# Optimization experiments

Measured on AMD Instinct MI355X. Metric: run time of the kernel, lower is better.

## Reference

```python
import jax, jax.numpy as jnp
import numpy as np

D = 1024
N_PASSES = 2


def _hadamard(d):
    # Sylvester construction: d must be a power of 2
    H = np.array([[1.0]], dtype=np.float32)
    while H.shape[0] < d:
        H = np.block([[H, H], [H, -H]])
    return H


def setup_inputs() -> dict:
    key = jax.random.key(0)
    kx, ks = jax.random.split(key)
    x = jax.random.normal(kx, (8, 8192, D), dtype=jnp.float32)
    # random +/-1 sign vectors, one per pass
    signs = jnp.where(jax.random.bernoulli(ks, 0.5, (N_PASSES, D)), 1.0, -1.0).astype(jnp.float32)
    h_mat = jnp.asarray(_hadamard(D))  # unnormalized Walsh-Hadamard matrix [D, D]
    return {"x": x, "signs": signs, "h_mat": h_mat}


def reference(x, signs, h_mat):
    # Cascaded SRHT: (sign flip -> WHT -> scale by 1/sqrt(d)) x n_passes
    d = x.shape[-1]
    scale = 1.0 / jnp.sqrt(jnp.asarray(d, dtype=x.dtype))
    out = x
    for i in range(N_PASSES):
        out = (out * signs[i]) @ h_mat * scale
    return out
```

## Files before the change

### kernel.cpp

```cpp
#include <hip/hip_runtime.h>

#define DD 1024

__device__ __forceinline__ void fwht16(float (&v)[16]) {
  #pragma unroll
  for (int h = 1; h < 16; h <<= 1) {
    #pragma unroll
    for (int i = 0; i < 16; ++i) {
      if (!(i & h)) {
        float a = v[i], b = v[i | h];
        v[i]     = a + b;
        v[i | h] = a - b;
      }
    }
  }
}

__device__ __forceinline__ void shfl_stage(float (&v)[16], int mask, int lane) {
  const float sgn = (lane & mask) ? -1.0f : 1.0f;
  #pragma unroll
  for (int j = 0; j < 16; ++j) {
    float o = __shfl_xor(v[j], mask, 64);
    v[j] = fmaf(sgn, v[j], o);
  }
}

__global__ __launch_bounds__(256) void srht_kernel(
    const float* __restrict__ x,
    const float* __restrict__ signs,
    float* __restrict__ out)
{
  __shared__ float lds[4][DD + DD / 32];
  const int lane = threadIdx.x & 63;
  const int wv   = threadIdx.x >> 6;
  const long row = (long)blockIdx.x * 4 + wv;

  const float* __restrict__ xr = x + row * DD;
  float* __restrict__ orow     = out + row * DD;
  const float* __restrict__ s0 = signs;
  const float* __restrict__ s1 = signs + DD;
  float* buf = lds[wv];

  float v[16];

  {
    const float4* xp = (const float4*)(xr + 16 * lane);
    const float4* sp = (const float4*)(s0 + 16 * lane);
    #pragma unroll
    for (int c = 0; c < 4; ++c) {
      float4 a = xp[c], s = sp[c];
      v[4 * c + 0] = a.x * s.x;
      v[4 * c + 1] = a.y * s.y;
      v[4 * c + 2] = a.z * s.z;
      v[4 * c + 3] = a.w * s.w;
    }
  }

  fwht16(v);
  shfl_stage(v, 1, lane);
  shfl_stage(v, 2, lane);

  {
    const int wb = 16 * lane + (lane >> 1);
    #pragma unroll
    for (int j = 0; j < 16; ++j) buf[wb + j] = v[j];
  }
  __syncthreads();
  {
    const int rb = lane + (lane >> 5);
    #pragma unroll
    for (int k = 0; k < 16; ++k) v[k] = buf[rb + 66 * k];
  }
  fwht16(v);

  #pragma unroll
  for (int k = 0; k < 16; ++k)
    v[k] *= s1[lane + 64 * k] * 0.03125f;

  fwht16(v);
  __syncthreads();
  {
    const int wb = lane + (lane >> 5);
    #pragma unroll
    for (int k = 0; k < 16; ++k) buf[wb + 66 * k] = v[k];
  }
  __syncthreads();
  {
    const int rb = 16 * lane + (lane >> 1);
    #pragma unroll
    for (int j = 0; j < 16; ++j) v[j] = buf[rb + j];
  }
  shfl_stage(v, 1, lane);
  shfl_stage(v, 2, lane);
  fwht16(v);

  {
    float4* op = (float4*)(orow + 16 * lane);
    #pragma unroll
    for (int c = 0; c < 4; ++c) {
      float4 r;
      r.x = v[4 * c + 0] * 0.03125f;
      r.y = v[4 * c + 1] * 0.03125f;
      r.z = v[4 * c + 2] * 0.03125f;
      r.w = v[4 * c + 3] * 0.03125f;
      op[c] = r;
    }
  }
}

extern "C" void kernel_launch(void* const* d_in, const int* in_sizes, int n_in,
                              void* d_out, int out_size, void* d_ws, size_t ws_size,
                              hipStream_t stream) {
  const float* x     = (const float*)d_in[0];
  const float* signs = (const float*)d_in[1];
  float* out         = (float*)d_out;

  const int rows   = in_sizes[0] / DD;
  const int blocks = rows / 4;

  hipLaunchKernelGGL(srht_kernel, dim3(blocks), dim3(256), 0, stream,
                     x, signs, out);
}
```

Baseline: 122.9 us.

## Use DPP/swizzle cross-lane WHT, bitmask signs, and persistent double-buffered waves

After: 442.8 us. 260% more time.

```diff
diff --git a/kernel.cpp b/kernel.cpp
--- a/kernel.cpp
+++ b/kernel.cpp
@@ -1,6 +1,15 @@
 #include <hip/hip_runtime.h>
+#include <stdint.h>
 
 #define DD 1024
+
+typedef float f32x4 __attribute__((ext_vector_type(4)));
+
+template <int CTRL>
+__device__ __forceinline__ float xdpp(float v) {
+  return __int_as_float(__builtin_amdgcn_update_dpp(
+      0, __float_as_int(v), CTRL, 0xF, 0xF, true));
+}
 
 __device__ __forceinline__ void fwht16(float (&v)[16]) {
   #pragma unroll
@@ -16,95 +25,137 @@
   }
 }
 
-__device__ __forceinline__ void shfl_stage(float (&v)[16], int mask, int lane) {
-  const float sgn = (lane & mask) ? -1.0f : 1.0f;
+__device__ __forceinline__ void wht1024(float (&v)[16],
+    float sg1, float sg2, float sg4, float sg8, float sg16, float sg32) {
+  fwht16(v);
   #pragma unroll
   for (int j = 0; j < 16; ++j) {
-    float o = __shfl_xor(v[j], mask, 64);
-    v[j] = fmaf(sgn, v[j], o);
+    float o = xdpp<0xB1>(v[j]);
+    v[j] = fmaf(sg1, v[j], o);
+  }
+  #pragma unroll
+  for (int j = 0; j < 16; ++j) {
+    float o = xdpp<0x4E>(v[j]);
+    v[j] = fmaf(sg2, v[j], o);
+  }
+  #pragma unroll
+  for (int j = 0; j < 16; ++j) {
+    float o = xdpp<0x141>(xdpp<0x1B>(v[j]));
+    v[j] = fmaf(sg4, v[j], o);
+  }
+  #pragma unroll
+  for (int j = 0; j < 16; ++j) {
+    float o = xdpp<0x140>(xdpp<0x141>(v[j]));
+    v[j] = fmaf(sg8, v[j], o);
+  }
+  #pragma unroll
+  for (int j = 0; j < 16; ++j) {
+    float o = __int_as_float(
+        __builtin_amdgcn_ds_swizzle(__float_as_int(v[j]), 0x401F));
+    v[j] = fmaf(sg16, v[j], o);
+  }
+  #pragma unroll
+  for (int j = 0; j < 16; ++j) {
+    float o = __shfl_xor(v[j], 32, 64);
+    v[j] = fmaf(sg32, v[j], o);
   }
 }
 
-__global__ __launch_bounds__(256) void srht_kernel(
-    const float* __restrict__ x,
-    const float* __restrict__ signs,
-    float* __restrict__ out)
+__device__ __forceinline__ void load_row(const float* __restrict__ x, long r,
+                                         int lane, float (&v)[16]) {
+  const f32x4* p = (const f32x4*)(x + r * (long)DD + 16 * lane);
+  #pragma unroll
+  for (int c = 0; c < 4; ++c) {
+    f32x4 a = p[c];
+    v[4 * c + 0] = a.x; v[4 * c + 1] = a.y;
+    v[4 * c + 2] = a.z; v[4 * c + 3] = a.w;
+  }
+}
+
+__device__ __forceinline__ void proc_store(float (&v)[16],
+    float* __restrict__ out, long r, int lane, uint32_t s0p, uint32_t s1p,
+    float sg1, float sg2, float sg4, float sg8, float sg16, float sg32) {
+  #pragma unroll
+  for (int j = 0; j < 16; ++j)
+    v[j] = __uint_as_float(__float_as_uint(v[j]) ^
+                           ((s0p << (31 - j)) & 0x80000000u));
+  wht1024(v, sg1, sg2, sg4, sg8, sg16, sg32);
+  #pragma unroll
+  for (int j = 0; j < 16; ++j)
+    v[j] = __uint_as_float(__float_as_uint(v[j]) ^
+                           ((s1p << (31 - j)) & 0x80000000u));
+  wht1024(v, sg1, sg2, sg4, sg8, sg16, sg32);
+
+  f32x4* op = (f32x4*)(out + r * (long)DD + 16 * lane);
+  const float S = 1.0f / 1024.0f;
+  #pragma unroll
+  for (int c = 0; c < 4; ++c) {
+    f32x4 o4;
+    o4.x = v[4 * c + 0] * S; o4.y = v[4 * c + 1] * S;
+    o4.z = v[4 * c + 2] * S; o4.w = v[4 * c + 3] * S;
+    op[c] = o4;
+  }
+}
+
+__global__ __launch_bounds__(256, 8) void srht_kernel(
+    const float* __restrict__ x, const float* __restrict__ signs,
+    float* __restrict__ out, int iters, int wstride, int rows)
 {
-  __shared__ float lds[4][DD + DD / 32];
   const int lane = threadIdx.x & 63;
-  const int wv   = threadIdx.x >> 6;
-  const long row = (long)blockIdx.x * 4 + wv;
+  const int gw   = blockIdx.x * 4 + (threadIdx.x >> 6);
 
-  const float* __restrict__ xr = x + row * DD;
-  float* __restrict__ orow     = out + row * DD;
-  const float* __restrict__ s0 = signs;
-  const float* __restrict__ s1 = signs + DD;
-  float* buf = lds[wv];
-
-  float v[16];
-
+  uint32_t s0p = 0, s1p = 0;
   {
-    const float4* xp = (const float4*)(xr + 16 * lane);
-    const float4* sp = (const float4*)(s0 + 16 * lane);
+    const f32x4* sp0 = (const f32x4*)(signs + 16 * lane);
+    const f32x4* sp1 = (const f32x4*)(signs + DD + 16 * lane);
     #pragma unroll
     for (int c = 0; c < 4; ++c) {
-      float4 a = xp[c], s = sp[c];
-      v[4 * c + 0] = a.x * s.x;
-      v[4 * c + 1] = a.y * s.y;
-      v[4 * c + 2] = a.z * s.z;
-      v[4 * c + 3] = a.w * s.w;
+      f32x4 a = sp0[c], b = sp1[c];
+      s0p |= (__float_as_uint(a.x) >> 31) << (4 * c + 0);
+      s0p |= (__float_as_uint(a.y) >> 31) << (4 * c + 1);
+      s0p |= (__float_as_uint(a.z) >> 31) << (4 * c + 2);
+      s0p |= (__float_as_uint(a.w) >> 31) << (4 * c + 3);
+      s1p |= (__float_as_uint(b.x) >> 31) << (4 * c + 0);
+      s1p |= (__float_as_uint(b.y) >> 31) << (4 * c + 1);
+      s1p |= (__float_as_uint(b.z) >> 31) << (4 * c + 2);
+      s1p |= (__float_as_uint(b.w) >> 31) << (4 * c + 3);
+    }
+  }
+  const float sg1  = (lane & 1)  ? -1.f : 1.f;
+  const float sg2  = (lane & 2)  ? -1.f : 1.f;
+  const float sg4  = (lane & 4)  ? -1.f : 1.f;
+  const float sg8  = (lane & 8)  ? -1.f : 1.f;
+  const float sg16 = (lane & 16) ? -1.f : 1.f;
+  const float sg32 = (lane & 32) ? -1.f : 1.f;
+
+  float vA[16], vB[16];
+  long rA = gw;
+  long rB = gw + (long)wstride;
+  if (rB >= rows) rB = gw;
+  load_row(x, rA, lane, vA);
+  load_row(x, rB, lane, vB);
+
+  for (int it = 0; it < iters; it += 2) {
+    proc_store(vA, out, rA, lane, s0p, s1p, sg1, sg2, sg4, sg8, sg16, sg32);
+    {
+      long rn = rA + 2L * wstride;
+      if (rn >= rows) rn = gw;
+      load_row(x, rn, lane, vA);
+      rA = rn;
+    }
+    if (it + 1 < iters) {
+      proc_store(vB, out, rB, lane, s0p, s1p, sg1, sg2, sg4, sg8, sg16, sg32);
+      long rn = rB + 2L * wstride;
+      if (rn >= rows) rn = gw;
+      load_row(x, rn, lane, vB);
+      rB = rn;
     }
   }
 
-  fwht16(v);
-  shfl_stage(v, 1, lane);
-  shfl_stage(v, 2, lane);
-
-  {
-    const int wb = 16 * lane + (lane >> 1);
-    #pragma unroll
-    for (int j = 0; j < 16; ++j) buf[wb + j] = v[j];
-  }
-  __syncthreads();
-  {
-    const int rb = lane + (lane >> 5);
-    #pragma unroll
-    for (int k = 0; k < 16; ++k) v[k] = buf[rb + 66 * k];
-  }
-  fwht16(v);
-
-  #pragma unroll
-  for (int k = 0; k < 16; ++k)
-    v[k] *= s1[lane + 64 * k] * 0.03125f;
-
-  fwht16(v);
-  __syncthreads();
-  {
-    const int wb = lane + (lane >> 5);
-    #pragma unroll
-    for (int k = 0; k < 16; ++k) buf[wb + 66 * k] = v[k];
-  }
-  __syncthreads();
-  {
-    const int rb = 16 * lane + (lane >> 1);
-    #pragma unroll
-    for (int j = 0; j < 16; ++j) v[j] = buf[rb + j];
-  }
-  shfl_stage(v, 1, lane);
-  shfl_stage(v, 2, lane);
-  fwht16(v);
-
-  {
-    float4* op = (float4*)(orow + 16 * lane);
-    #pragma unroll
-    for (int c = 0; c < 4; ++c) {
-      float4 r;
-      r.x = v[4 * c + 0] * 0.03125f;
-      r.y = v[4 * c + 1] * 0.03125f;
-      r.z = v[4 * c + 2] * 0.03125f;
-      r.w = v[4 * c + 3] * 0.03125f;
-      op[c] = r;
-    }
+  long rt = (long)iters * wstride + gw;
+  if (rt < rows) {
+    load_row(x, rt, lane, vA);
+    proc_store(vA, out, rt, lane, s0p, s1p, sg1, sg2, sg4, sg8, sg16, sg32);
   }
 }
 
@@ -116,8 +167,10 @@
   float* out         = (float*)d_out;
 
   const int rows   = in_sizes[0] / DD;
-  const int blocks = rows / 4;
+  const int blocks = 2048;
+  const int waves  = blocks * 4;
+  const int iters  = rows / waves;
 
   hipLaunchKernelGGL(srht_kernel, dim3(blocks), dim3(256), 0, stream,
-                     x, signs, out);
+                     x, signs, out, iters, waves, rows);
 }
```
